# Performance work log

Hardware: AMD Instinct MI355X
Metric: run time of the kernel (lower is better)

## Reference

```python
import jax, jax.numpy as jnp
import numpy as np

B, M, C = 2048, 64, 256

def setup_inputs() -> dict:
    key = jax.random.key(0)
    k1, k2, k3 = jax.random.split(key, 3)
    node_features = jax.random.normal(k1, (B, M, C), dtype=jnp.float32)
    # torch nn.Linear(C, C, bias=False): weight [out=C, in=C], kaiming-uniform-ish scale
    lim_w = 1.0 / np.sqrt(C)
    W = jax.random.uniform(k2, (C, C), dtype=jnp.float32, minval=-lim_w, maxval=lim_w)
    # attn_mlp: Linear(2C, 1, bias=False) -> weight [1, 2C]; store flat [2C]
    lim_a = 1.0 / np.sqrt(2 * C)
    attn_w = jax.random.uniform(k3, (2 * C,), dtype=jnp.float32, minval=-lim_a, maxval=lim_a)
    return {"node_features": node_features, "W": W, "attn_w": attn_w}

def reference(node_features, W, attn_w):
    # h = W(node_features): [B, M, C]
    h = jnp.einsum('bmc,oc->bmo', node_features, W)
    # attn_mlp(cat[h_i, h_j]) == h_i @ a_i + h_j @ a_j (split weight) -> broadcast add
    a_i, a_j = attn_w[:C], attn_w[C:]
    s_i = h @ a_i  # [B, M] score contribution of row node
    s_j = h @ a_j  # [B, M] score contribution of col node
    e = jax.nn.leaky_relu(s_i[:, :, None] + s_j[:, None, :], negative_slope=0.2)  # [B,M,M]
    attn = jax.nn.softmax(e, axis=2)
    updated = jnp.einsum('bij,bjc->bic', attn, h)  # bmm
    return jax.nn.relu(updated)
```

## Files before the change

kernel.cpp:

```cpp
#include <hip/hip_runtime.h>
#include <stdint.h>
#include <stddef.h>


#define NB 2048
#define MM 64
#define CC 256

typedef __attribute__((ext_vector_type(4))) float    f32x4;
typedef __attribute__((ext_vector_type(8))) _Float16 h16x8;
typedef __attribute__((ext_vector_type(4))) _Float16 h16x4;

#define XH 0
#define XL 32768
#define AT 65536
#define ATL 73728

__device__ __forceinline__ f32x4 mfma16(h16x8 a, h16x8 b, f32x4 c) {
    return __builtin_amdgcn_mfma_f32_16x16x32_f16(a, b, c, 0, 0, 0);
}

__global__ void prep_w(const float* __restrict__ W,
                       _Float16* __restrict__ Wh, _Float16* __restrict__ Wl) {
    int t = blockIdx.x * 256 + threadIdx.x;
    f32x4 v = ((const f32x4*)W)[t];
    h16x4 hv, lv;
#pragma unroll
    for (int e = 0; e < 4; ++e) {
        _Float16 h = (_Float16)v[e];
        hv[e] = h;
        lv[e] = (_Float16)(v[e] - (float)h);
    }
    ((h16x4*)Wh)[t] = hv;
    ((h16x4*)Wl)[t] = lv;
}

__global__ __launch_bounds__(256, 2)
void gat_kernel(const float* __restrict__ x, const float* __restrict__ aw,
                const _Float16* __restrict__ Wh, const _Float16* __restrict__ Wl,
                float* __restrict__ out) {
    extern __shared__ char smem[];
    const int b    = blockIdx.x;
    const int tid  = threadIdx.x;
    const int w    = tid >> 6;
    const int lane = tid & 63;
    const int l15  = lane & 15;
    const int lq   = lane >> 4;

    const float* xb = x + (size_t)b * (MM * CC);
#pragma unroll
    for (int it = 0; it < 8; ++it) {
        int r  = it * 8 + (tid >> 5);
        int c8 = tid & 31;
        const float* src = xb + r * CC + c8 * 8;
        f32x4 v0 = *(const f32x4*)(src);
        f32x4 v1 = *(const f32x4*)(src + 4);
        h16x8 hv, lv;
#pragma unroll
        for (int e = 0; e < 4; ++e) {
            float f0 = v0[e], f1 = v1[e];
            _Float16 h0 = (_Float16)f0; hv[e]     = h0; lv[e]     = (_Float16)(f0 - (float)h0);
            _Float16 h1 = (_Float16)f1; hv[4 + e] = h1; lv[4 + e] = (_Float16)(f1 - (float)h1);
        }
        int byte = r * 512 + ((c8 ^ (r & 7)) * 16);
        *(h16x8*)(smem + XH + byte) = hv;
        *(h16x8*)(smem + XL + byte) = lv;
    }
    __syncthreads();

    f32x4 acc[4][4] = {};
    {
        h16x8 Bh[2][4], Bl[2][4];
#pragma unroll
        for (int nt = 0; nt < 4; ++nt) {
            int col = w * 64 + nt * 16 + l15;
            Bh[0][nt] = *(const h16x8*)(Wh + col * CC + lq * 8);
            Bl[0][nt] = *(const h16x8*)(Wl + col * CC + lq * 8);
        }
#pragma unroll
        for (int ks = 0; ks < 8; ++ks) {
            int cur = ks & 1, nxt = cur ^ 1;
            if (ks < 7) {
#pragma unroll
                for (int nt = 0; nt < 4; ++nt) {
                    int col = w * 64 + nt * 16 + l15;
                    Bh[nxt][nt] = *(const h16x8*)(Wh + col * CC + (ks + 1) * 32 + lq * 8);
                    Bl[nxt][nt] = *(const h16x8*)(Wl + col * CC + (ks + 1) * 32 + lq * 8);
                }
            }
#pragma unroll
            for (int mt = 0; mt < 4; ++mt) {
                int r = mt * 16 + l15;
                int g = (((ks * 4 + lq) ^ (r & 7)) * 16);
                h16x8 Ah = *(const h16x8*)(smem + XH + r * 512 + g);
                h16x8 Al = *(const h16x8*)(smem + XL + r * 512 + g);
#pragma unroll
                for (int nt = 0; nt < 4; ++nt) {
                    acc[mt][nt] = mfma16(Al, Bh[cur][nt], acc[mt][nt]);
                    acc[mt][nt] = mfma16(Ah, Bl[cur][nt], acc[mt][nt]);
                    acc[mt][nt] = mfma16(Ah, Bh[cur][nt], acc[mt][nt]);
                }
            }
        }
    }

    float* sparti = (float*)(smem + AT);
    float* spartj = (float*)(smem + AT + 1024);
    float* sfini  = (float*)(smem + AT + 2048);
    float* sfinj  = (float*)(smem + AT + 2304);
    {
        float ai[4], aj[4];
#pragma unroll
        for (int nt = 0; nt < 4; ++nt) {
            int col = w * 64 + nt * 16 + l15;
            ai[nt] = aw[col];
            aj[nt] = aw[256 + col];
        }
#pragma unroll
        for (int mt = 0; mt < 4; ++mt) {
#pragma unroll
            for (int rg = 0; rg < 4; ++rg) {
                float s1 = 0.f, s2 = 0.f;
#pragma unroll
                for (int nt = 0; nt < 4; ++nt) {
                    float v = acc[mt][nt][rg];
                    s1 += v * ai[nt];
                    s2 += v * aj[nt];
                }
                s1 += __shfl_xor(s1, 1);  s2 += __shfl_xor(s2, 1);
                s1 += __shfl_xor(s1, 2);  s2 += __shfl_xor(s2, 2);
                s1 += __shfl_xor(s1, 4);  s2 += __shfl_xor(s2, 4);
                s1 += __shfl_xor(s1, 8);  s2 += __shfl_xor(s2, 8);
                if (l15 == 0) {
                    int row = mt * 16 + lq * 4 + rg;
                    sparti[w * 64 + row] = s1;
                    spartj[w * 64 + row] = s2;
                }
            }
        }
    }
    __syncthreads();

#pragma unroll
    for (int mt = 0; mt < 4; ++mt) {
#pragma unroll
        for (int nt = 0; nt < 4; ++nt) {
            h16x4 hh, ll;
#pragma unroll
            for (int rg = 0; rg < 4; ++rg) {
                float f = acc[mt][nt][rg];
                _Float16 h = (_Float16)f;
                hh[rg] = h;
                ll[rg] = (_Float16)(f - (float)h);
            }
            int c    = w * 64 + nt * 16 + l15;
            int jb   = mt * 16 + lq * 4;
            int byte = c * 128 + (((jb >> 3) ^ (c & 7)) * 16) + (jb & 7) * 2;
            *(h16x4*)(smem + XH + byte) = hh;
            *(h16x4*)(smem + XL + byte) = ll;
        }
    }
    if (tid < 128) {
        int row = tid & 63;
        float* sp = (tid < 64) ? sparti : spartj;
        float v = sp[row] + sp[64 + row] + sp[128 + row] + sp[192 + row];
        ((tid < 64) ? sfini : sfinj)[row] = v;
    }
    __syncthreads();

    {
        int i  = w * 16 + l15;
        int jb = lq * 16;
        float siv = sfini[i];
        float p[16];
        float mx = -1e30f;
#pragma unroll
        for (int t4 = 0; t4 < 4; ++t4) {
            f32x4 sv = *(const f32x4*)(sfinj + jb + t4 * 4);
#pragma unroll
            for (int e = 0; e < 4; ++e) {
                float ev = siv + sv[e];
                ev = ev > 0.f ? ev : 0.2f * ev;
                p[t4 * 4 + e] = ev;
                mx = fmaxf(mx, ev);
            }
        }
        mx = fmaxf(mx, __shfl_xor(mx, 16));
        mx = fmaxf(mx, __shfl_xor(mx, 32));
        float sum = 0.f;
#pragma unroll
        for (int t = 0; t < 16; ++t) { p[t] = __expf(p[t] - mx); sum += p[t]; }
        sum += __shfl_xor(sum, 16);
        sum += __shfl_xor(sum, 32);
        float inv = 1.0f / sum;
        __syncthreads();
        h16x8 ph0, ph1, pl0, pl1;
#pragma unroll
        for (int t = 0; t < 8; ++t) {
            float f0 = p[t] * inv;     _Float16 h0 = (_Float16)f0;
            ph0[t] = h0; pl0[t] = (_Float16)(f0 - (float)h0);
            float f1 = p[8 + t] * inv; _Float16 h1 = (_Float16)f1;
            ph1[t] = h1; pl1[t] = (_Float16)(f1 - (float)h1);
        }
        int base = AT + i * 128;
        int g0 = (((2 * lq)     ^ (i & 7)) * 16);
        int g1 = (((2 * lq + 1) ^ (i & 7)) * 16);
        *(h16x8*)(smem + base + g0) = ph0;
        *(h16x8*)(smem + base + g1) = ph1;
        *(h16x8*)(smem + (ATL - AT) + base + g0) = pl0;
        *(h16x8*)(smem + (ATL - AT) + base + g1) = pl1;
    }
    __syncthreads();

    f32x4 acc2[4][4] = {};
#pragma unroll
    for (int ks = 0; ks < 2; ++ks) {
        h16x8 Ah[4], Al[4], Bh2[4], Bl2[4];
#pragma unroll
        for (int mt = 0; mt < 4; ++mt) {
            int r = mt * 16 + l15;
            int g = (((ks * 4 + lq) ^ (r & 7)) * 16);
            Ah[mt] = *(const h16x8*)(smem + AT  + r * 128 + g);
            Al[mt] = *(const h16x8*)(smem + ATL + r * 128 + g);
        }
#pragma unroll
        for (int nt = 0; nt < 4; ++nt) {
            int c = w * 64 + nt * 16 + l15;
            int g = (((ks * 4 + lq) ^ (c & 7)) * 16);
            Bh2[nt] = *(const h16x8*)(smem + XH + c * 128 + g);
            Bl2[nt] = *(const h16x8*)(smem + XL + c * 128 + g);
        }
#pragma unroll
        for (int mt = 0; mt < 4; ++mt) {
#pragma unroll
            for (int nt = 0; nt < 4; ++nt) {
                acc2[mt][nt] = mfma16(Al[mt], Bh2[nt], acc2[mt][nt]);
                acc2[mt][nt] = mfma16(Ah[mt], Bl2[nt], acc2[mt][nt]);
                acc2[mt][nt] = mfma16(Ah[mt], Bh2[nt], acc2[mt][nt]);
            }
        }
    }

    float* ob = out + (size_t)b * (MM * CC);
#pragma unroll
    for (int mt = 0; mt < 4; ++mt) {
#pragma unroll
        for (int nt = 0; nt < 4; ++nt) {
            int col = w * 64 + nt * 16 + l15;
#pragma unroll
            for (int rg = 0; rg < 4; ++rg) {
                int row = mt * 16 + lq * 4 + rg;
                ob[row * CC + col] = fmaxf(acc2[mt][nt][rg], 0.f);
            }
        }
    }
}

extern "C" void kernel_launch(void* const* d_in, const int* in_sizes, int n_in,
                              void* d_out, int out_size, void* d_ws, size_t ws_size,
                              hipStream_t stream) {
    (void)in_sizes; (void)n_in; (void)out_size; (void)ws_size;
    const float* x  = (const float*)d_in[0];
    const float* W  = (const float*)d_in[1];
    const float* aw = (const float*)d_in[2];
    float* out = (float*)d_out;

    _Float16* Wh = (_Float16*)d_ws;
    _Float16* Wl = Wh + 65536;

    (void)hipFuncSetAttribute((const void*)gat_kernel,
                              hipFuncAttributeMaxDynamicSharedMemorySize, 81920);

    prep_w<<<64, 256, 0, stream>>>(W, Wh, Wl);
    gat_kernel<<<NB, 256, 81920, stream>>>(x, aw, Wh, Wl, out);
}
```

Measured before the change: 303.3 us.

## Use 512 threads per block and stage output through LDS for coalesced stores

Doubles the block to 8 waves, so each wave owns 32 output columns instead of 64. This halves the accumulator registers per thread and raises the number of waves per CU. The softmax is remapped to 8 lanes per row, and the score partials now reduce over 8 waves. The final ReLU output is written to padded shared memory and then stored to global memory as coalesced 16-byte vectors instead of scattered scalar stores. In exchange it adds a barrier, and each block still uses 80KB of LDS, which limits how many blocks fit per CU.

```diff
diff --git a/kernel.cpp b/kernel.cpp
--- a/kernel.cpp
+++ b/kernel.cpp
@@ -11,10 +11,15 @@
 typedef __attribute__((ext_vector_type(8))) _Float16 h16x8;
 typedef __attribute__((ext_vector_type(4))) _Float16 h16x4;
 
-#define XH 0
-#define XL 32768
-#define AT 65536
+#define XH  0
+#define XL  32768
+#define AT  65536
 #define ATL 73728
+#define SP_I 65536
+#define SP_J 67584
+#define SF_I 69632
+#define SF_J 69888
+#define OSTR 1040
 
 __device__ __forceinline__ f32x4 mfma16(h16x8 a, h16x8 b, f32x4 c) {
     return __builtin_amdgcn_mfma_f32_16x16x32_f16(a, b, c, 0, 0, 0);
@@ -35,7 +40,7 @@
     ((h16x4*)Wl)[t] = lv;
 }
 
-__global__ __launch_bounds__(256, 2)
+__global__ __launch_bounds__(512, 4)
 void gat_kernel(const float* __restrict__ x, const float* __restrict__ aw,
                 const _Float16* __restrict__ Wh, const _Float16* __restrict__ Wl,
                 float* __restrict__ out) {
@@ -48,81 +53,77 @@
     const int lq   = lane >> 4;
 
     const float* xb = x + (size_t)b * (MM * CC);
-#pragma unroll
-    for (int it = 0; it < 8; ++it) {
-        int r  = it * 8 + (tid >> 5);
-        int c8 = tid & 31;
-        const float* src = xb + r * CC + c8 * 8;
-        f32x4 v0 = *(const f32x4*)(src);
-        f32x4 v1 = *(const f32x4*)(src + 4);
-        h16x8 hv, lv;
-#pragma unroll
-        for (int e = 0; e < 4; ++e) {
-            float f0 = v0[e], f1 = v1[e];
-            _Float16 h0 = (_Float16)f0; hv[e]     = h0; lv[e]     = (_Float16)(f0 - (float)h0);
-            _Float16 h1 = (_Float16)f1; hv[4 + e] = h1; lv[4 + e] = (_Float16)(f1 - (float)h1);
-        }
-        int byte = r * 512 + ((c8 ^ (r & 7)) * 16);
-        *(h16x8*)(smem + XH + byte) = hv;
-        *(h16x8*)(smem + XL + byte) = lv;
-    }
-    __syncthreads();
-
-    f32x4 acc[4][4] = {};
     {
-        h16x8 Bh[2][4], Bl[2][4];
-#pragma unroll
-        for (int nt = 0; nt < 4; ++nt) {
-            int col = w * 64 + nt * 16 + l15;
-            Bh[0][nt] = *(const h16x8*)(Wh + col * CC + lq * 8);
-            Bl[0][nt] = *(const h16x8*)(Wl + col * CC + lq * 8);
-        }
-#pragma unroll
-        for (int ks = 0; ks < 8; ++ks) {
-            int cur = ks & 1, nxt = cur ^ 1;
-            if (ks < 7) {
-#pragma unroll
-                for (int nt = 0; nt < 4; ++nt) {
-                    int col = w * 64 + nt * 16 + l15;
-                    Bh[nxt][nt] = *(const h16x8*)(Wh + col * CC + (ks + 1) * 32 + lq * 8);
-                    Bl[nxt][nt] = *(const h16x8*)(Wl + col * CC + (ks + 1) * 32 + lq * 8);
-                }
-            }
-#pragma unroll
-            for (int mt = 0; mt < 4; ++mt) {
-                int r = mt * 16 + l15;
-                int g = (((ks * 4 + lq) ^ (r & 7)) * 16);
-                h16x8 Ah = *(const h16x8*)(smem + XH + r * 512 + g);
-                h16x8 Al = *(const h16x8*)(smem + XL + r * 512 + g);
-#pragma unroll
-                for (int nt = 0; nt < 4; ++nt) {
-                    acc[mt][nt] = mfma16(Al, Bh[cur][nt], acc[mt][nt]);
-                    acc[mt][nt] = mfma16(Ah, Bl[cur][nt], acc[mt][nt]);
-                    acc[mt][nt] = mfma16(Ah, Bh[cur][nt], acc[mt][nt]);
-                }
-            }
-        }
-    }
-
-    float* sparti = (float*)(smem + AT);
-    float* spartj = (float*)(smem + AT + 1024);
-    float* sfini  = (float*)(smem + AT + 2048);
-    float* sfinj  = (float*)(smem + AT + 2304);
+        int r  = tid >> 3;
+        int g0 = tid & 7;
+#pragma unroll
+        for (int it = 0; it < 4; ++it) {
+            int g8 = g0 + it * 8;
+            const float* src = xb + r * CC + g8 * 8;
+            f32x4 v0 = *(const f32x4*)(src);
+            f32x4 v1 = *(const f32x4*)(src + 4);
+            h16x8 hv, lv;
+#pragma unroll
+            for (int e = 0; e < 4; ++e) {
+                float f0 = v0[e], f1 = v1[e];
+                _Float16 h0 = (_Float16)f0; hv[e]   = h0; lv[e]   = (_Float16)(f0 - (float)h0);
+                _Float16 h1 = (_Float16)f1; hv[4+e] = h1; lv[4+e] = (_Float16)(f1 - (float)h1);
+            }
+            int byte = r * 512 + ((g8 ^ (r & 7)) * 16);
+            *(h16x8*)(smem + XH + byte) = hv;
+            *(h16x8*)(smem + XL + byte) = lv;
+        }
+    }
+
+    h16x8 Bh[2][2], Bl[2][2];
+    float ai[2], aj[2];
+#pragma unroll
+    for (int nt = 0; nt < 2; ++nt) {
+        int col = w * 32 + nt * 16 + l15;
+        Bh[0][nt] = *(const h16x8*)(Wh + col * CC + lq * 8);
+        Bl[0][nt] = *(const h16x8*)(Wl + col * CC + lq * 8);
+        ai[nt] = aw[col];
+        aj[nt] = aw[256 + col];
+    }
+    __syncthreads();
+
+    f32x4 acc[4][2] = {};
+#pragma unroll
+    for (int ks = 0; ks < 8; ++ks) {
+        int cur = ks & 1, nxt = cur ^ 1;
+        if (ks < 7) {
+#pragma unroll
+            for (int nt = 0; nt < 2; ++nt) {
+                int col = w * 32 + nt * 16 + l15;
+                Bh[nxt][nt] = *(const h16x8*)(Wh + col * CC + (ks + 1) * 32 + lq * 8);
+                Bl[nxt][nt] = *(const h16x8*)(Wl + col * CC + (ks + 1) * 32 + lq * 8);
+            }
+        }
+#pragma unroll
+        for (int mt = 0; mt < 4; ++mt) {
+            int r = mt * 16 + l15;
+            int g = (((ks * 4 + lq) ^ (r & 7)) * 16);
+            h16x8 Ah = *(const h16x8*)(smem + XH + r * 512 + g);
+            h16x8 Al = *(const h16x8*)(smem + XL + r * 512 + g);
+#pragma unroll
+            for (int nt = 0; nt < 2; ++nt) {
+                acc[mt][nt] = mfma16(Al, Bh[cur][nt], acc[mt][nt]);
+                acc[mt][nt] = mfma16(Ah, Bl[cur][nt], acc[mt][nt]);
+                acc[mt][nt] = mfma16(Ah, Bh[cur][nt], acc[mt][nt]);
+            }
+        }
+    }
+
     {
-        float ai[4], aj[4];
-#pragma unroll
-        for (int nt = 0; nt < 4; ++nt) {
-            int col = w * 64 + nt * 16 + l15;
-            ai[nt] = aw[col];
-            aj[nt] = aw[256 + col];
-        }
+        float* sparti = (float*)(smem + SP_I);
+        float* spartj = (float*)(smem + SP_J);
 #pragma unroll
         for (int mt = 0; mt < 4; ++mt) {
 #pragma unroll
             for (int rg = 0; rg < 4; ++rg) {
                 float s1 = 0.f, s2 = 0.f;
 #pragma unroll
-                for (int nt = 0; nt < 4; ++nt) {
+                for (int nt = 0; nt < 2; ++nt) {
                     float v = acc[mt][nt][rg];
                     s1 += v * ai[nt];
                     s2 += v * aj[nt];
@@ -144,7 +145,7 @@
 #pragma unroll
     for (int mt = 0; mt < 4; ++mt) {
 #pragma unroll
-        for (int nt = 0; nt < 4; ++nt) {
+        for (int nt = 0; nt < 2; ++nt) {
             h16x4 hh, ll;
 #pragma unroll
             for (int rg = 0; rg < 4; ++rg) {
@@ -153,7 +154,7 @@
                 hh[rg] = h;
                 ll[rg] = (_Float16)(f - (float)h);
             }
-            int c    = w * 64 + nt * 16 + l15;
+            int c    = w * 32 + nt * 16 + l15;
             int jb   = mt * 16 + lq * 4;
             int byte = c * 128 + (((jb >> 3) ^ (c & 7)) * 16) + (jb & 7) * 2;
             *(h16x4*)(smem + XH + byte) = hh;
@@ -162,70 +163,72 @@
     }
     if (tid < 128) {
         int row = tid & 63;
-        float* sp = (tid < 64) ? sparti : spartj;
-        float v = sp[row] + sp[64 + row] + sp[128 + row] + sp[192 + row];
-        ((tid < 64) ? sfini : sfinj)[row] = v;
+        const float* sp = (tid < 64) ? (const float*)(smem + SP_I)
+                                     : (const float*)(smem + SP_J);
+        float v = 0.f;
+#pragma unroll
+        for (int k = 0; k < 8; ++k) v += sp[k * 64 + row];
+        float* dst = (tid < 64) ? (float*)(smem + SF_I) : (float*)(smem + SF_J);
+        dst[row] = v;
     }
     __syncthreads();
 
     {
-        int i  = w * 16 + l15;
-        int jb = lq * 16;
+        const float* sfini = (const float*)(smem + SF_I);
+        const float* sfinj = (const float*)(smem + SF_J);
+        int i  = w * 8 + (lane >> 3);
+        int jc = (lane & 7) * 8;
         float siv = sfini[i];
-        float p[16];
+        f32x4 sv0 = *(const f32x4*)(sfinj + jc);
+        f32x4 sv1 = *(const f32x4*)(sfinj + jc + 4);
+        float p[8];
         float mx = -1e30f;
 #pragma unroll
-        for (int t4 = 0; t4 < 4; ++t4) {
-            f32x4 sv = *(const f32x4*)(sfinj + jb + t4 * 4);
-#pragma unroll
-            for (int e = 0; e < 4; ++e) {
-                float ev = siv + sv[e];
-                ev = ev > 0.f ? ev : 0.2f * ev;
-                p[t4 * 4 + e] = ev;
-                mx = fmaxf(mx, ev);
-            }
-        }
-        mx = fmaxf(mx, __shfl_xor(mx, 16));
-        mx = fmaxf(mx, __shfl_xor(mx, 32));
+        for (int e = 0; e < 4; ++e) {
+            float e0 = siv + sv0[e]; e0 = e0 > 0.f ? e0 : 0.2f * e0;
+            float e1 = siv + sv1[e]; e1 = e1 > 0.f ? e1 : 0.2f * e1;
+            p[e] = e0; p[4 + e] = e1;
+            mx = fmaxf(mx, fmaxf(e0, e1));
+        }
+        mx = fmaxf(mx, __shfl_xor(mx, 1));
+        mx = fmaxf(mx, __shfl_xor(mx, 2));
+        mx = fmaxf(mx, __shfl_xor(mx, 4));
         float sum = 0.f;
 #pragma unroll
-        for (int t = 0; t < 16; ++t) { p[t] = __expf(p[t] - mx); sum += p[t]; }
-        sum += __shfl_xor(sum, 16);
-        sum += __shfl_xor(sum, 32);
+        for (int t = 0; t < 8; ++t) { p[t] = __expf(p[t] - mx); sum += p[t]; }
+        sum += __shfl_xor(sum, 1);
+        sum += __shfl_xor(sum, 2);
+        sum += __shfl_xor(sum, 4);
         float inv = 1.0f / sum;
         __syncthreads();
-        h16x8 ph0, ph1, pl0, pl1;
+        h16x8 ph, pl;
 #pragma unroll
         for (int t = 0; t < 8; ++t) {
-            float f0 = p[t] * inv;     _Float16 h0 = (_Float16)f0;
-            ph0[t] = h0; pl0[t] = (_Float16)(f0 - (float)h0);
-            float f1 = p[8 + t] * inv; _Float16 h1 = (_Float16)f1;
-            ph1[t] = h1; pl1[t] = (_Float16)(f1 - (float)h1);
-        }
-        int base = AT + i * 128;
-        int g0 = (((2 * lq)     ^ (i & 7)) * 16);
-        int g1 = (((2 * lq + 1) ^ (i & 7)) * 16);
-        *(h16x8*)(smem + base + g0) = ph0;
-        *(h16x8*)(smem + base + g1) = ph1;
-        *(h16x8*)(smem + (ATL - AT) + base + g0) = pl0;
-        *(h16x8*)(smem + (ATL - AT) + base + g1) = pl1;
-    }
-    __syncthreads();
-
-    f32x4 acc2[4][4] = {};
+            float f = p[t] * inv;
+            _Float16 h = (_Float16)f;
+            ph[t] = h;
+            pl[t] = (_Float16)(f - (float)h);
+        }
+        int byte = i * 128 + (((lane & 7) ^ (i & 7)) * 16);
+        *(h16x8*)(smem + AT  + byte) = ph;
+        *(h16x8*)(smem + ATL + byte) = pl;
+    }
+    __syncthreads();
+
+    f32x4 acc2[4][2] = {};
 #pragma unroll
     for (int ks = 0; ks < 2; ++ks) {
-        h16x8 Ah[4], Al[4], Bh2[4], Bl2[4];
-#pragma unroll
-        for (int mt = 0; mt < 4; ++mt) {
-            int r = mt * 16 + l15;
-            int g = (((ks * 4 + lq) ^ (r & 7)) * 16);
-            Ah[mt] = *(const h16x8*)(smem + AT  + r * 128 + g);
-            Al[mt] = *(const h16x8*)(smem + ATL + r * 128 + g);
-        }
-#pragma unroll
-        for (int nt = 0; nt < 4; ++nt) {
-            int c = w * 64 + nt * 16 + l15;
+        h16x8 Ah2[4], Al2[4], Bh2[2], Bl2[2];
+#pragma unroll
+        for (int mt = 0; mt < 4; ++mt) {
+            int i = mt * 16 + l15;
+            int g = (((ks * 4 + lq) ^ (i & 7)) * 16);
+            Ah2[mt] = *(const h16x8*)(smem + AT  + i * 128 + g);
+            Al2[mt] = *(const h16x8*)(smem + ATL + i * 128 + g);
+        }
+#pragma unroll
+        for (int nt = 0; nt < 2; ++nt) {
+            int c = w * 32 + nt * 16 + l15;
             int g = (((ks * 4 + lq) ^ (c & 7)) * 16);
             Bh2[nt] = *(const h16x8*)(smem + XH + c * 128 + g);
             Bl2[nt] = *(const h16x8*)(smem + XL + c * 128 + g);
@@ -233,26 +236,37 @@
 #pragma unroll
         for (int mt = 0; mt < 4; ++mt) {
 #pragma unroll
-            for (int nt = 0; nt < 4; ++nt) {
-                acc2[mt][nt] = mfma16(Al[mt], Bh2[nt], acc2[mt][nt]);
-                acc2[mt][nt] = mfma16(Ah[mt], Bl2[nt], acc2[mt][nt]);
-                acc2[mt][nt] = mfma16(Ah[mt], Bh2[nt], acc2[mt][nt]);
-            }
-        }
-    }
-
-    float* ob = out + (size_t)b * (MM * CC);
+            for (int nt = 0; nt < 2; ++nt) {
+                acc2[mt][nt] = mfma16(Al2[mt], Bh2[nt], acc2[mt][nt]);
+                acc2[mt][nt] = mfma16(Ah2[mt], Bl2[nt], acc2[mt][nt]);
+                acc2[mt][nt] = mfma16(Ah2[mt], Bh2[nt], acc2[mt][nt]);
+            }
+        }
+    }
+    __syncthreads();
+
 #pragma unroll
     for (int mt = 0; mt < 4; ++mt) {
 #pragma unroll
-        for (int nt = 0; nt < 4; ++nt) {
-            int col = w * 64 + nt * 16 + l15;
+        for (int nt = 0; nt < 2; ++nt) {
+            int col = w * 32 + nt * 16 + l15;
 #pragma unroll
             for (int rg = 0; rg < 4; ++rg) {
                 int row = mt * 16 + lq * 4 + rg;
-                ob[row * CC + col] = fmaxf(acc2[mt][nt][rg], 0.f);
-            }
-        }
+                *(float*)(smem + row * OSTR + col * 4) =
+                    fmaxf(acc2[mt][nt][rg], 0.f);
+            }
+        }
+    }
+    __syncthreads();
+    float* ob = out + (size_t)b * (MM * CC);
+#pragma unroll
+    for (int it = 0; it < 8; ++it) {
+        int idx = it * 512 + tid;
+        int row = idx >> 6;
+        int c4  = idx & 63;
+        f32x4 v = *(const f32x4*)(smem + row * OSTR + c4 * 16);
+        *(f32x4*)(ob + idx * 4) = v;
     }
 }
 
@@ -272,5 +286,5 @@
                               hipFuncAttributeMaxDynamicSharedMemorySize, 81920);
 
     prep_w<<<64, 256, 0, stream>>>(W, Wh, Wl);
-    gat_kernel<<<NB, 256, 81920, stream>>>(x, aw, Wh, Wl, out);
-}
+    gat_kernel<<<NB, 512, 81920, stream>>>(x, aw, Wh, Wl, out);
+}
```

Measured after the change: 290.4 us. 4.3% less time.
